# Optimization experiments

Measured on AMD Instinct MI355X. Metric: run time of the kernel, lower is better.

Reference implementation:

```python
import jax, jax.numpy as jnp
import numpy as np

N = 50000
IN_CH = 256
HID = 256
E = 800000


def setup_inputs() -> dict:
    key = jax.random.key(0)
    ks = jax.random.split(key, 12)
    s = 1.0 / np.sqrt(HID)
    return {
        "x": jax.random.normal(ks[0], (N, IN_CH), jnp.float32),
        "edge_index": jax.random.randint(ks[1], (2, E), 0, N, dtype=jnp.int64),
        "prev_embedding": jax.random.normal(ks[2], (N, HID), jnp.float32),
        "W1": jax.random.normal(ks[3], (IN_CH, HID), jnp.float32) / np.sqrt(IN_CH),
        "b1": jnp.zeros((HID,), jnp.float32),
        "W2": jax.random.normal(ks[4], (HID, HID), jnp.float32) * s,
        "b2": jnp.zeros((HID,), jnp.float32),
        "gWw": jax.random.normal(ks[5], (HID, HID), jnp.float32) * s,
        "gWb": jnp.zeros((HID,), jnp.float32),
        "gUw": jax.random.normal(ks[6], (HID, HID), jnp.float32) * s,
        "gUb": jnp.zeros((HID,), jnp.float32),
    }


def _gcn_conv(x, W, b, src, dst, norm):
    # PyG GCNConv: h = x @ W; out[i] = sum_j norm_ij * h[j]; + bias
    h = x @ W
    msg = h[src] * norm[:, None]  # [E+N, H]
    out = jax.ops.segment_sum(msg, dst, num_segments=N)
    return out + b


def _norm_and_loops(edge_index):
    loop = jnp.arange(N, dtype=edge_index.dtype)
    src = jnp.concatenate([edge_index[0], loop])
    dst = jnp.concatenate([edge_index[1], loop])
    deg = jax.ops.segment_sum(jnp.ones_like(dst, dtype=jnp.float32), dst, num_segments=N)
    dinv = jnp.where(deg > 0, jax.lax.rsqrt(deg), 0.0)
    norm = dinv[src] * dinv[dst]
    return src, dst, norm


def reference(x, edge_index, prev_embedding, W1, b1, W2, b2, gWw, gWb, gUw, gUb):
    src, dst, norm = _norm_and_loops(edge_index)
    h = jax.nn.relu(_gcn_conv(x, W1, b1, src, dst, norm))
    h_t = _gcn_conv(h, W2, b2, src, dst, norm)
    alpha = jax.nn.sigmoid(h_t @ gWw + gWb + prev_embedding @ gUw + gUb)
    h_tilde = alpha * h_t + (1.0 - alpha) * prev_embedding
    return (h_tilde, h_t)
```

## Files before the change

### kernel.cpp

```cpp
#include <hip/hip_runtime.h>
#include <hip/hip_bf16.h>
#include <math.h>

#define HIDC 256
#define LSTR 40

typedef short short8 __attribute__((ext_vector_type(8)));
typedef float f32x4 __attribute__((ext_vector_type(4)));

__device__ __forceinline__ ushort f2bf_rne(float f) {
    uint u = __float_as_uint(f);
    u += 0x7FFF + ((u >> 16) & 1);
    return (ushort)(u >> 16);
}
__device__ __forceinline__ float bf2f(ushort h) {
    return __uint_as_float(((uint)h) << 16);
}


__global__ void fill_i_kernel(int* __restrict__ p, int v, int n) {
    int i = blockIdx.x * 256 + threadIdx.x;
    if (i < n) p[i] = v;
}

__global__ void deg_kernel(const int* __restrict__ dst, int* __restrict__ deg, int E) {
    int e = blockIdx.x * 256 + threadIdx.x;
    if (e < E) atomicAdd(&deg[dst[e]], 1);
}

__global__ void rsqrt_kernel(const int* __restrict__ deg, float* __restrict__ dinv, int n) {
    int i = blockIdx.x * 256 + threadIdx.x;
    if (i < n) dinv[i] = rsqrtf((float)(deg[i] + 1));
}


__device__ __forceinline__ int block_incl_scan(int v, int tid) {
#pragma unroll
    for (int off = 1; off < 64; off <<= 1) {
        int t = __shfl_up(v, off);
        if ((tid & 63) >= off) v += t;
    }
    __shared__ int wt[4];
    if ((tid & 63) == 63) wt[tid >> 6] = v;
    __syncthreads();
    int wid = tid >> 6;
    for (int w = 0; w < wid; w++) v += wt[w];
    __syncthreads();
    return v;
}

__global__ void scan_a_kernel(const int* __restrict__ deg, int* __restrict__ row_start,
                              int* __restrict__ blocksum, int N) {
    int tid = threadIdx.x;
    int i = blockIdx.x * 256 + tid;
    int v = (i < N) ? deg[i] : 0;
    int incl = block_incl_scan(v, tid);
    if (i < N) row_start[i + 1] = incl;
    if (tid == 255) blocksum[blockIdx.x] = incl;
}

__global__ void scan_b_kernel(int* __restrict__ blocksum, int nb) {
    int tid = threadIdx.x;
    int v = (tid < nb) ? blocksum[tid] : 0;
    int incl = block_incl_scan(v, tid);
    if (tid < nb) blocksum[tid] = incl;
}

__global__ void scan_c_kernel(int* __restrict__ row_start, int* __restrict__ cursor,
                              const int* __restrict__ blocksum, int N) {
    int b = blockIdx.x;
    int i = b * 256 + threadIdx.x;
    int add = (b > 0) ? blocksum[b - 1] : 0;
    if (i < N) {
        int v = row_start[i + 1] + add;
        row_start[i + 1] = v;
        cursor[i + 1] = v;
    }
    if (b == 0 && threadIdx.x == 0) { row_start[0] = 0; cursor[0] = 0; }
}

__global__ void scatter_kernel(const int* __restrict__ src, const int* __restrict__ dst,
                               const float* __restrict__ dinv, int* __restrict__ cursor,
                               int* __restrict__ csr_src, float* __restrict__ csr_w, int E) {
    int e = blockIdx.x * 256 + threadIdx.x;
    if (e < E) {
        int s = src[e], d = dst[e];
        int pos = atomicAdd(&cursor[d], 1);
        csr_src[pos] = s;
        csr_w[pos] = dinv[s] * dinv[d];
    }
}


__global__ void prep_bt_kernel(const float* __restrict__ B, ushort* __restrict__ Bt) {
    int n = blockIdx.x, k = threadIdx.x;
    Bt[n * 256 + k] = f2bf_rne(B[k * 256 + n]);
}

__global__ void prep_gate_bt_kernel(const float* __restrict__ gWw, const float* __restrict__ gUw,
                                    ushort* __restrict__ Bth, ushort* __restrict__ Btl) {
    int n = blockIdx.x, k = threadIdx.x;
    float v1 = gWw[k * 256 + n];
    uint u1 = __float_as_uint(v1);
    Bth[n * 512 + k] = (ushort)(u1 >> 16);
    Btl[n * 512 + k] = f2bf_rne(v1 - __uint_as_float(u1 & 0xFFFF0000u));
    float v2 = gUw[k * 256 + n];
    uint u2 = __float_as_uint(v2);
    Bth[n * 512 + 256 + k] = (ushort)(u2 >> 16);
    Btl[n * 512 + 256 + k] = f2bf_rne(v2 - __uint_as_float(u2 & 0xFFFF0000u));
}


__global__ __launch_bounds__(256, 4) void gemm_bf16_kernel(
    const float* __restrict__ A, const ushort* __restrict__ Bt,
    ushort* __restrict__ C, int M)
{
    __shared__ __align__(16) ushort As[64 * LSTR];
    __shared__ __align__(16) ushort Bs[128 * LSTR];
    const int tl = threadIdx.x;
    const int lane = tl & 63, wave = tl >> 6;
    const int wm = (wave & 1) * 32, wn = (wave >> 1) * 64;
    const int bm = blockIdx.x * 64, bn = blockIdx.y * 128;

    const int arA = tl >> 2;
    const int kqA = (tl & 3) * 8;
    const int arB = tl >> 1;
    const int kqB = (tl & 1) * 16;
    const bool aok = (bm + arA) < M;

    f32x4 acc[2][4] = {};

    for (int k0 = 0; k0 < 256; k0 += 32) {
        {
            const float* ap = A + (size_t)(bm + arA) * HIDC + k0 + kqA;
            float4 v0 = aok ? *(const float4*)(ap)     : make_float4(0.f, 0.f, 0.f, 0.f);
            float4 v1 = aok ? *(const float4*)(ap + 4) : make_float4(0.f, 0.f, 0.f, 0.f);
            ushort4 h0, h1;
            h0.x = f2bf_rne(v0.x); h0.y = f2bf_rne(v0.y); h0.z = f2bf_rne(v0.z); h0.w = f2bf_rne(v0.w);
            h1.x = f2bf_rne(v1.x); h1.y = f2bf_rne(v1.y); h1.z = f2bf_rne(v1.z); h1.w = f2bf_rne(v1.w);
            *(ushort4*)&As[arA * LSTR + kqA]     = h0;
            *(ushort4*)&As[arA * LSTR + kqA + 4] = h1;
        }
        {
            const ushort* bp = Bt + (size_t)(bn + arB) * 256 + k0 + kqB;
            *(uint4*)&Bs[arB * LSTR + kqB]     = *(const uint4*)bp;
            *(uint4*)&Bs[arB * LSTR + kqB + 8] = *(const uint4*)(bp + 8);
        }
        __syncthreads();
        const int fr = lane & 15, koff = (lane >> 4) * 8;
        short8 af[2], bfv[4];
#pragma unroll
        for (int t = 0; t < 2; t++)
            af[t]  = *(const short8*)&As[(wm + t * 16 + fr) * LSTR + koff];
#pragma unroll
        for (int t = 0; t < 4; t++)
            bfv[t] = *(const short8*)&Bs[(wn + t * 16 + fr) * LSTR + koff];
#pragma unroll
        for (int mt = 0; mt < 2; mt++)
#pragma unroll
            for (int nt = 0; nt < 4; nt++)
                acc[mt][nt] = __builtin_amdgcn_mfma_f32_16x16x32_bf16(af[mt], bfv[nt], acc[mt][nt], 0, 0, 0);
        __syncthreads();
    }

    const int row4 = (lane >> 4) * 4, coln = lane & 15;
#pragma unroll
    for (int mt = 0; mt < 2; mt++)
#pragma unroll
        for (int r = 0; r < 4; r++) {
            int m = bm + wm + mt * 16 + row4 + r;
            if (m < M) {
#pragma unroll
                for (int nt = 0; nt < 4; nt++) {
                    int n = bn + wn + nt * 16 + coln;
                    C[(size_t)m * HIDC + n] = f2bf_rne(acc[mt][nt][r]);
                }
            }
        }
}


__global__ __launch_bounds__(256, 4) void gemm_bf16A_kernel(
    const ushort* __restrict__ A, const ushort* __restrict__ Bt,
    ushort* __restrict__ C, int M)
{
    __shared__ __align__(16) ushort As[64 * LSTR];
    __shared__ __align__(16) ushort Bs[128 * LSTR];
    const int tl = threadIdx.x;
    const int lane = tl & 63, wave = tl >> 6;
    const int wm = (wave & 1) * 32, wn = (wave >> 1) * 64;
    const int bm = blockIdx.x * 64, bn = blockIdx.y * 128;

    const int arA = tl >> 2;
    const int kqA = (tl & 3) * 8;
    const int arB = tl >> 1;
    const int kqB = (tl & 1) * 16;
    const bool aok = (bm + arA) < M;

    f32x4 acc[2][4] = {};

    for (int k0 = 0; k0 < 256; k0 += 32) {
        {
            const ushort* ap = A + (size_t)(bm + arA) * HIDC + k0 + kqA;
            uint2 z = make_uint2(0u, 0u);
            *(uint2*)&As[arA * LSTR + kqA]     = aok ? *(const uint2*)ap       : z;
            *(uint2*)&As[arA * LSTR + kqA + 4] = aok ? *(const uint2*)(ap + 4) : z;
        }
        {
            const ushort* bp = Bt + (size_t)(bn + arB) * 256 + k0 + kqB;
            *(uint4*)&Bs[arB * LSTR + kqB]     = *(const uint4*)bp;
            *(uint4*)&Bs[arB * LSTR + kqB + 8] = *(const uint4*)(bp + 8);
        }
        __syncthreads();
        const int fr = lane & 15, koff = (lane >> 4) * 8;
        short8 af[2], bfv[4];
#pragma unroll
        for (int t = 0; t < 2; t++)
            af[t]  = *(const short8*)&As[(wm + t * 16 + fr) * LSTR + koff];
#pragma unroll
        for (int t = 0; t < 4; t++)
            bfv[t] = *(const short8*)&Bs[(wn + t * 16 + fr) * LSTR + koff];
#pragma unroll
        for (int mt = 0; mt < 2; mt++)
#pragma unroll
            for (int nt = 0; nt < 4; nt++)
                acc[mt][nt] = __builtin_amdgcn_mfma_f32_16x16x32_bf16(af[mt], bfv[nt], acc[mt][nt], 0, 0, 0);
        __syncthreads();
    }

    const int row4 = (lane >> 4) * 4, coln = lane & 15;
#pragma unroll
    for (int mt = 0; mt < 2; mt++)
#pragma unroll
        for (int r = 0; r < 4; r++) {
            int m = bm + wm + mt * 16 + row4 + r;
            if (m < M) {
#pragma unroll
                for (int nt = 0; nt < 4; nt++) {
                    int n = bn + wn + nt * 16 + coln;
                    C[(size_t)m * HIDC + n] = f2bf_rne(acc[mt][nt][r]);
                }
            }
        }
}


__global__ __launch_bounds__(256, 4) void gate_kernel(
    const float* __restrict__ ht, const float* __restrict__ prev,
    const ushort* __restrict__ Bth, const ushort* __restrict__ Btl,
    const float* __restrict__ gWb, const float* __restrict__ gUb,
    float* __restrict__ out, int M)
{
    __shared__ __align__(16) ushort Ash[64 * LSTR];
    __shared__ __align__(16) ushort Asl[64 * LSTR];
    __shared__ __align__(16) ushort Bsh[128 * LSTR];
    __shared__ __align__(16) ushort Bsl[128 * LSTR];
    const int tl = threadIdx.x;
    const int lane = tl & 63, wave = tl >> 6;
    const int wm = (wave & 1) * 32, wn = (wave >> 1) * 64;
    const int bm = blockIdx.x * 64, bn = blockIdx.y * 128;

    const int arA = tl >> 2;
    const int kqA = (tl & 3) * 8;
    const int arB = tl >> 1;
    const int kqB = (tl & 1) * 16;
    const bool aok = (bm + arA) < M;

    f32x4 acc[2][4] = {};

    for (int k0 = 0; k0 < 512; k0 += 32) {
        {
            const float* srcA = (k0 < 256) ? ht : prev;
            const float* ap = srcA + (size_t)(bm + arA) * HIDC + (k0 & 255) + kqA;
            float4 v0 = aok ? *(const float4*)(ap)     : make_float4(0.f, 0.f, 0.f, 0.f);
            float4 v1 = aok ? *(const float4*)(ap + 4) : make_float4(0.f, 0.f, 0.f, 0.f);
            float vv[8] = {v0.x, v0.y, v0.z, v0.w, v1.x, v1.y, v1.z, v1.w};
            ushort hp[8], lp[8];
#pragma unroll
            for (int q = 0; q < 8; q++) {
                uint u = __float_as_uint(vv[q]);
                hp[q] = (ushort)(u >> 16);
                lp[q] = f2bf_rne(vv[q] - __uint_as_float(u & 0xFFFF0000u));
            }
            *(ushort4*)&Ash[arA * LSTR + kqA]     = make_ushort4(hp[0], hp[1], hp[2], hp[3]);
            *(ushort4*)&Ash[arA * LSTR + kqA + 4] = make_ushort4(hp[4], hp[5], hp[6], hp[7]);
            *(ushort4*)&Asl[arA * LSTR + kqA]     = make_ushort4(lp[0], lp[1], lp[2], lp[3]);
            *(ushort4*)&Asl[arA * LSTR + kqA + 4] = make_ushort4(lp[4], lp[5], lp[6], lp[7]);
        }
        {
            const ushort* bph = Bth + (size_t)(bn + arB) * 512 + k0 + kqB;
            const ushort* bpl = Btl + (size_t)(bn + arB) * 512 + k0 + kqB;
            *(uint4*)&Bsh[arB * LSTR + kqB]     = *(const uint4*)bph;
            *(uint4*)&Bsh[arB * LSTR + kqB + 8] = *(const uint4*)(bph + 8);
            *(uint4*)&Bsl[arB * LSTR + kqB]     = *(const uint4*)bpl;
            *(uint4*)&Bsl[arB * LSTR + kqB + 8] = *(const uint4*)(bpl + 8);
        }
        __syncthreads();
        const int fr = lane & 15, koff = (lane >> 4) * 8;
        short8 afh[2], afl[2], bfh[4], bfl[4];
#pragma unroll
        for (int t = 0; t < 2; t++) {
            afh[t] = *(const short8*)&Ash[(wm + t * 16 + fr) * LSTR + koff];
            afl[t] = *(const short8*)&Asl[(wm + t * 16 + fr) * LSTR + koff];
        }
#pragma unroll
        for (int t = 0; t < 4; t++) {
            bfh[t] = *(const short8*)&Bsh[(wn + t * 16 + fr) * LSTR + koff];
            bfl[t] = *(const short8*)&Bsl[(wn + t * 16 + fr) * LSTR + koff];
        }
#pragma unroll
        for (int mt = 0; mt < 2; mt++)
#pragma unroll
            for (int nt = 0; nt < 4; nt++) {
                acc[mt][nt] = __builtin_amdgcn_mfma_f32_16x16x32_bf16(afh[mt], bfh[nt], acc[mt][nt], 0, 0, 0);
                acc[mt][nt] = __builtin_amdgcn_mfma_f32_16x16x32_bf16(afh[mt], bfl[nt], acc[mt][nt], 0, 0, 0);
                acc[mt][nt] = __builtin_amdgcn_mfma_f32_16x16x32_bf16(afl[mt], bfh[nt], acc[mt][nt], 0, 0, 0);
            }
        __syncthreads();
    }

    const int row4 = (lane >> 4) * 4, coln = lane & 15;
#pragma unroll
    for (int mt = 0; mt < 2; mt++)
#pragma unroll
        for (int r = 0; r < 4; r++) {
            int m = bm + wm + mt * 16 + row4 + r;
            if (m < M) {
#pragma unroll
                for (int nt = 0; nt < 4; nt++) {
                    int n = bn + wn + nt * 16 + coln;
                    size_t idx = (size_t)m * HIDC + n;
                    float g = acc[mt][nt][r] + gWb[n] + gUb[n];
                    float alpha = 1.f / (1.f + expf(-g));
                    out[idx] = alpha * ht[idx] + (1.f - alpha) * prev[idx];
                }
            }
        }
}


__global__ __launch_bounds__(256) void csr_agg_kernel(
    const ushort* __restrict__ hm, const int* __restrict__ row_start,
    const int* __restrict__ csr_src, const float* __restrict__ csr_w,
    const float* __restrict__ dinv, const float* __restrict__ bias,
    float* __restrict__ outf, ushort* __restrict__ outb, int do_relu, int N)
{
    const int wave = threadIdx.x >> 6, lane = threadIdx.x & 63;
    const int i = blockIdx.x * 4 + wave;
    if (i >= N) return;
    const int c = lane * 4;

    const float di = dinv[i];
    const float s2 = di * di;
    ushort4 sv = *(const ushort4*)(hm + (size_t)i * HIDC + c);
    float a0 = s2 * bf2f(sv.x), a1 = s2 * bf2f(sv.y);
    float a2 = s2 * bf2f(sv.z), a3 = s2 * bf2f(sv.w);

    const int b0 = row_start[i], b1 = row_start[i + 1];
    int t = b0;
    for (; t + 4 <= b1; t += 4) {
        int   i0 = csr_src[t],     i1 = csr_src[t + 1];
        int   i2 = csr_src[t + 2], i3 = csr_src[t + 3];
        float w0 = csr_w[t],       w1 = csr_w[t + 1];
        float w2 = csr_w[t + 2],   w3 = csr_w[t + 3];
        ushort4 v0 = *(const ushort4*)(hm + (size_t)i0 * HIDC + c);
        ushort4 v1 = *(const ushort4*)(hm + (size_t)i1 * HIDC + c);
        ushort4 v2 = *(const ushort4*)(hm + (size_t)i2 * HIDC + c);
        ushort4 v3 = *(const ushort4*)(hm + (size_t)i3 * HIDC + c);
        a0 += w0 * bf2f(v0.x); a1 += w0 * bf2f(v0.y); a2 += w0 * bf2f(v0.z); a3 += w0 * bf2f(v0.w);
        a0 += w1 * bf2f(v1.x); a1 += w1 * bf2f(v1.y); a2 += w1 * bf2f(v1.z); a3 += w1 * bf2f(v1.w);
        a0 += w2 * bf2f(v2.x); a1 += w2 * bf2f(v2.y); a2 += w2 * bf2f(v2.z); a3 += w2 * bf2f(v2.w);
        a0 += w3 * bf2f(v3.x); a1 += w3 * bf2f(v3.y); a2 += w3 * bf2f(v3.z); a3 += w3 * bf2f(v3.w);
    }
    for (; t < b1; ++t) {
        int s_ = csr_src[t];
        float w = csr_w[t];
        ushort4 v = *(const ushort4*)(hm + (size_t)s_ * HIDC + c);
        a0 += w * bf2f(v.x); a1 += w * bf2f(v.y); a2 += w * bf2f(v.z); a3 += w * bf2f(v.w);
    }

    float4 bb = *(const float4*)(bias + c);
    a0 += bb.x; a1 += bb.y; a2 += bb.z; a3 += bb.w;
    if (do_relu) {
        a0 = fmaxf(a0, 0.f); a1 = fmaxf(a1, 0.f);
        a2 = fmaxf(a2, 0.f); a3 = fmaxf(a3, 0.f);
    }
    if (outb) {
        ushort4 o;
        o.x = f2bf_rne(a0); o.y = f2bf_rne(a1);
        o.z = f2bf_rne(a2); o.w = f2bf_rne(a3);
        *(ushort4*)(outb + (size_t)i * HIDC + c) = o;
    } else {
        *(float4*)(outf + (size_t)i * HIDC + c) = make_float4(a0, a1, a2, a3);
    }
}


extern "C" void kernel_launch(void* const* d_in, const int* in_sizes, int n_in,
                              void* d_out, int out_size, void* d_ws, size_t ws_size,
                              hipStream_t stream) {
    const float* x    = (const float*)d_in[0];
    const int*   ei   = (const int*)d_in[1];
    const float* prev = (const float*)d_in[2];
    const float* W1   = (const float*)d_in[3];
    const float* b1   = (const float*)d_in[4];
    const float* W2   = (const float*)d_in[5];
    const float* b2   = (const float*)d_in[6];
    const float* gWw  = (const float*)d_in[7];
    const float* gWb  = (const float*)d_in[8];
    const float* gUw  = (const float*)d_in[9];
    const float* gUb  = (const float*)d_in[10];

    const int N = in_sizes[0] / HIDC;
    const int E = in_sizes[1] / 2;
    const int* src = ei;
    const int* dst = ei + E;

    float* out  = (float*)d_out;
    float* out1 = out;
    float* ht   = out + (size_t)N * HIDC;
    ushort* hbf = (ushort*)out1;

    float* ws = (float*)d_ws;
    size_t o = 0;
    auto take = [&](size_t n) { size_t r = o; o += (n + 63) & ~(size_t)63; return r; };
    float*  dinv    = ws + take(N);
    int*    degi    = (int*)(ws + take(N));
    int*    row_st  = (int*)(ws + take(N + 1));
    int*    cursor  = (int*)(ws + take(N + 1));
    int*    csr_src = (int*)(ws + take(E));
    float*  csr_w   = ws + take(E);
    ushort* Bt1     = (ushort*)(ws + take(256 * 256 / 2));
    ushort* Bt2     = (ushort*)(ws + take(256 * 256 / 2));
    ushort* Bth     = (ushort*)(ws + take(256 * 512 / 2));
    ushort* Btl     = (ushort*)(ws + take(256 * 512 / 2));
    ushort* hm      = (ushort*)(ws + take((size_t)N * HIDC / 2));

    const int nbN = (N + 255) / 256;
    const int nbE = (E + 255) / 256;
    dim3 ggrid((N + 63) / 64, 2);
    const int nbAgg = (N + 3) / 4;

    int* blocksum = (int*)csr_w;
    fill_i_kernel<<<nbN, 256, 0, stream>>>(degi, 0, N);
    deg_kernel<<<nbE, 256, 0, stream>>>(dst, degi, E);
    scan_a_kernel<<<nbN, 256, 0, stream>>>(degi, row_st, blocksum, N);
    scan_b_kernel<<<1, 256, 0, stream>>>(blocksum, nbN);
    scan_c_kernel<<<nbN, 256, 0, stream>>>(row_st, cursor, blocksum, N);
    rsqrt_kernel<<<nbN, 256, 0, stream>>>(degi, dinv, N);
    scatter_kernel<<<nbE, 256, 0, stream>>>(src, dst, dinv, cursor, csr_src, csr_w, E);

    prep_bt_kernel<<<256, 256, 0, stream>>>(W1, Bt1);
    prep_bt_kernel<<<256, 256, 0, stream>>>(W2, Bt2);
    prep_gate_bt_kernel<<<256, 256, 0, stream>>>(gWw, gUw, Bth, Btl);

    gemm_bf16_kernel<<<ggrid, 256, 0, stream>>>(x, Bt1, hm, N);
    csr_agg_kernel<<<nbAgg, 256, 0, stream>>>(hm, row_st, csr_src, csr_w, dinv, b1,
                                              nullptr, hbf, 1, N);

    gemm_bf16A_kernel<<<ggrid, 256, 0, stream>>>(hbf, Bt2, hm, N);
    csr_agg_kernel<<<nbAgg, 256, 0, stream>>>(hm, row_st, csr_src, csr_w, dinv, b2,
                                              ht, nullptr, 0, N);

    gate_kernel<<<ggrid, 256, 0, stream>>>(ht, prev, Bth, Btl, gWb, gUb, out1, N);

    (void)n_in; (void)out_size; (void)ws_size;
}
```

Baseline: 516.0 us.

## Drop LDS staging in GEMMs and pre-swizzle weights into MFMA fragment layout

All three GEMM kernels stop staging A and B tiles through shared memory. Each wave now loads its A fragments straight from global memory. B fragments come from a weight buffer that the prep kernels pre-arrange into the exact per-lane MFMA operand order, so the per-K-step __syncthreads and LDS traffic go away. The cost is redundant global/L2 reads: the two waves that share rows fetch the same A data, and the waves that share columns fetch the same B data. Latency hiding also now relies on occupancy, since there is no explicit double buffering.

```diff
diff --git a/kernel.cpp b/kernel.cpp
--- a/kernel.cpp
+++ b/kernel.cpp
@@ -3,7 +3,6 @@
 #include <math.h>
 
 #define HIDC 256
-#define LSTR 40
 
 typedef short short8 __attribute__((ext_vector_type(8)));
 typedef float f32x4 __attribute__((ext_vector_type(4)));
@@ -15,6 +14,24 @@
 }
 __device__ __forceinline__ float bf2f(ushort h) {
     return __uint_as_float(((uint)h) << 16);
+}
+
+__device__ __forceinline__ short8 pack8_rne(float4 a, float4 b) {
+    ushort h[8];
+    h[0] = f2bf_rne(a.x); h[1] = f2bf_rne(a.y); h[2] = f2bf_rne(a.z); h[3] = f2bf_rne(a.w);
+    h[4] = f2bf_rne(b.x); h[5] = f2bf_rne(b.y); h[6] = f2bf_rne(b.z); h[7] = f2bf_rne(b.w);
+    return *(short8*)h;
+}
+__device__ __forceinline__ void split8(float4 a, float4 b, short8& hi, short8& lo) {
+    float v[8] = {a.x, a.y, a.z, a.w, b.x, b.y, b.z, b.w};
+    ushort hh[8], ll[8];
+#pragma unroll
+    for (int q = 0; q < 8; q++) {
+        uint u = __float_as_uint(v[q]);
+        hh[q] = (ushort)(u >> 16);
+        ll[q] = f2bf_rne(v[q] - __uint_as_float(u & 0xFFFF0000u));
+    }
+    hi = *(short8*)hh; lo = *(short8*)ll;
 }
 
 
@@ -92,75 +109,65 @@
 }
 
 
-__global__ void prep_bt_kernel(const float* __restrict__ B, ushort* __restrict__ Bt) {
+__global__ void prep_bt_kernel(const float* __restrict__ B, ushort* __restrict__ BF) {
     int n = blockIdx.x, k = threadIdx.x;
-    Bt[n * 256 + k] = f2bf_rne(B[k * 256 + n]);
+    ushort v = f2bf_rne(B[k * 256 + n]);
+    int lane = ((k >> 3) & 3) * 16 + (n & 15);
+    int idx = ((n >> 4) * 4096) + ((k >> 5) * 512) + lane * 8 + (k & 7);
+    BF[idx] = v;
 }
 
 __global__ void prep_gate_bt_kernel(const float* __restrict__ gWw, const float* __restrict__ gUw,
-                                    ushort* __restrict__ Bth, ushort* __restrict__ Btl) {
-    int n = blockIdx.x, k = threadIdx.x;
-    float v1 = gWw[k * 256 + n];
-    uint u1 = __float_as_uint(v1);
-    Bth[n * 512 + k] = (ushort)(u1 >> 16);
-    Btl[n * 512 + k] = f2bf_rne(v1 - __uint_as_float(u1 & 0xFFFF0000u));
-    float v2 = gUw[k * 256 + n];
-    uint u2 = __float_as_uint(v2);
-    Bth[n * 512 + 256 + k] = (ushort)(u2 >> 16);
-    Btl[n * 512 + 256 + k] = f2bf_rne(v2 - __uint_as_float(u2 & 0xFFFF0000u));
+                                    ushort* __restrict__ BhF, ushort* __restrict__ BlF) {
+    int n = blockIdx.x, t = threadIdx.x;
+#pragma unroll
+    for (int p = 0; p < 2; p++) {
+        int k = p * 256 + t;
+        float v = (p ? gUw : gWw)[t * 256 + n];
+        uint u = __float_as_uint(v);
+        ushort hi = (ushort)(u >> 16);
+        ushort lo = f2bf_rne(v - __uint_as_float(u & 0xFFFF0000u));
+        int lane = ((k >> 3) & 3) * 16 + (n & 15);
+        int idx = ((n >> 4) * 8192) + ((k >> 5) * 512) + lane * 8 + (k & 7);
+        BhF[idx] = hi; BlF[idx] = lo;
+    }
 }
 
 
 __global__ __launch_bounds__(256, 4) void gemm_bf16_kernel(
-    const float* __restrict__ A, const ushort* __restrict__ Bt,
+    const float* __restrict__ A, const ushort* __restrict__ BF,
     ushort* __restrict__ C, int M)
 {
-    __shared__ __align__(16) ushort As[64 * LSTR];
-    __shared__ __align__(16) ushort Bs[128 * LSTR];
     const int tl = threadIdx.x;
     const int lane = tl & 63, wave = tl >> 6;
     const int wm = (wave & 1) * 32, wn = (wave >> 1) * 64;
     const int bm = blockIdx.x * 64, bn = blockIdx.y * 128;
-
-    const int arA = tl >> 2;
-    const int kqA = (tl & 3) * 8;
-    const int arB = tl >> 1;
-    const int kqB = (tl & 1) * 16;
-    const bool aok = (bm + arA) < M;
+    const int fr = lane & 15, kg = (lane >> 4) * 8;
+
+    const int r0 = bm + wm + fr, r1 = r0 + 16;
+    const bool ok0 = r0 < M, ok1 = r1 < M;
+    const float* a0 = A + (size_t)r0 * HIDC + kg;
+    const float* a1 = A + (size_t)r1 * HIDC + kg;
+    const ushort* bp = BF + (size_t)((bn + wn) >> 4) * 4096 + lane * 8;
 
     f32x4 acc[2][4] = {};
 
-    for (int k0 = 0; k0 < 256; k0 += 32) {
-        {
-            const float* ap = A + (size_t)(bm + arA) * HIDC + k0 + kqA;
-            float4 v0 = aok ? *(const float4*)(ap)     : make_float4(0.f, 0.f, 0.f, 0.f);
-            float4 v1 = aok ? *(const float4*)(ap + 4) : make_float4(0.f, 0.f, 0.f, 0.f);
-            ushort4 h0, h1;
-            h0.x = f2bf_rne(v0.x); h0.y = f2bf_rne(v0.y); h0.z = f2bf_rne(v0.z); h0.w = f2bf_rne(v0.w);
-            h1.x = f2bf_rne(v1.x); h1.y = f2bf_rne(v1.y); h1.z = f2bf_rne(v1.z); h1.w = f2bf_rne(v1.w);
-            *(ushort4*)&As[arA * LSTR + kqA]     = h0;
-            *(ushort4*)&As[arA * LSTR + kqA + 4] = h1;
-        }
-        {
-            const ushort* bp = Bt + (size_t)(bn + arB) * 256 + k0 + kqB;
-            *(uint4*)&Bs[arB * LSTR + kqB]     = *(const uint4*)bp;
-            *(uint4*)&Bs[arB * LSTR + kqB + 8] = *(const uint4*)(bp + 8);
-        }
-        __syncthreads();
-        const int fr = lane & 15, koff = (lane >> 4) * 8;
-        short8 af[2], bfv[4];
-#pragma unroll
-        for (int t = 0; t < 2; t++)
-            af[t]  = *(const short8*)&As[(wm + t * 16 + fr) * LSTR + koff];
-#pragma unroll
-        for (int t = 0; t < 4; t++)
-            bfv[t] = *(const short8*)&Bs[(wn + t * 16 + fr) * LSTR + koff];
-#pragma unroll
-        for (int mt = 0; mt < 2; mt++)
-#pragma unroll
-            for (int nt = 0; nt < 4; nt++)
-                acc[mt][nt] = __builtin_amdgcn_mfma_f32_16x16x32_bf16(af[mt], bfv[nt], acc[mt][nt], 0, 0, 0);
-        __syncthreads();
+    for (int kq = 0; kq < 8; kq++) {
+        float4 z = make_float4(0.f, 0.f, 0.f, 0.f);
+        float4 u0 = z, u1 = z, v0 = z, v1 = z;
+        if (ok0) { u0 = *(const float4*)(a0 + kq * 32); u1 = *(const float4*)(a0 + kq * 32 + 4); }
+        if (ok1) { v0 = *(const float4*)(a1 + kq * 32); v1 = *(const float4*)(a1 + kq * 32 + 4); }
+        short8 af0 = pack8_rne(u0, u1);
+        short8 af1 = pack8_rne(v0, v1);
+        short8 bfv[4];
+#pragma unroll
+        for (int nt = 0; nt < 4; nt++)
+            bfv[nt] = *(const short8*)(bp + ((size_t)nt * 8 + kq) * 512);
+#pragma unroll
+        for (int nt = 0; nt < 4; nt++) {
+            acc[0][nt] = __builtin_amdgcn_mfma_f32_16x16x32_bf16(af0, bfv[nt], acc[0][nt], 0, 0, 0);
+            acc[1][nt] = __builtin_amdgcn_mfma_f32_16x16x32_bf16(af1, bfv[nt], acc[1][nt], 0, 0, 0);
+        }
     }
 
     const int row4 = (lane >> 4) * 4, coln = lane & 15;
@@ -181,51 +188,36 @@
 
 
 __global__ __launch_bounds__(256, 4) void gemm_bf16A_kernel(
-    const ushort* __restrict__ A, const ushort* __restrict__ Bt,
+    const ushort* __restrict__ A, const ushort* __restrict__ BF,
     ushort* __restrict__ C, int M)
 {
-    __shared__ __align__(16) ushort As[64 * LSTR];
-    __shared__ __align__(16) ushort Bs[128 * LSTR];
     const int tl = threadIdx.x;
     const int lane = tl & 63, wave = tl >> 6;
     const int wm = (wave & 1) * 32, wn = (wave >> 1) * 64;
     const int bm = blockIdx.x * 64, bn = blockIdx.y * 128;
-
-    const int arA = tl >> 2;
-    const int kqA = (tl & 3) * 8;
-    const int arB = tl >> 1;
-    const int kqB = (tl & 1) * 16;
-    const bool aok = (bm + arA) < M;
+    const int fr = lane & 15, kg = (lane >> 4) * 8;
+
+    const int r0 = bm + wm + fr, r1 = r0 + 16;
+    const bool ok0 = r0 < M, ok1 = r1 < M;
+    const ushort* a0 = A + (size_t)r0 * HIDC + kg;
+    const ushort* a1 = A + (size_t)r1 * HIDC + kg;
+    const ushort* bp = BF + (size_t)((bn + wn) >> 4) * 4096 + lane * 8;
 
     f32x4 acc[2][4] = {};
 
-    for (int k0 = 0; k0 < 256; k0 += 32) {
-        {
-            const ushort* ap = A + (size_t)(bm + arA) * HIDC + k0 + kqA;
-            uint2 z = make_uint2(0u, 0u);
-            *(uint2*)&As[arA * LSTR + kqA]     = aok ? *(const uint2*)ap       : z;
-            *(uint2*)&As[arA * LSTR + kqA + 4] = aok ? *(const uint2*)(ap + 4) : z;
-        }
-        {
-            const ushort* bp = Bt + (size_t)(bn + arB) * 256 + k0 + kqB;
-            *(uint4*)&Bs[arB * LSTR + kqB]     = *(const uint4*)bp;
-            *(uint4*)&Bs[arB * LSTR + kqB + 8] = *(const uint4*)(bp + 8);
-        }
-        __syncthreads();
-        const int fr = lane & 15, koff = (lane >> 4) * 8;
-        short8 af[2], bfv[4];
-#pragma unroll
-        for (int t = 0; t < 2; t++)
-            af[t]  = *(const short8*)&As[(wm + t * 16 + fr) * LSTR + koff];
-#pragma unroll
-        for (int t = 0; t < 4; t++)
-            bfv[t] = *(const short8*)&Bs[(wn + t * 16 + fr) * LSTR + koff];
-#pragma unroll
-        for (int mt = 0; mt < 2; mt++)
-#pragma unroll
-            for (int nt = 0; nt < 4; nt++)
-                acc[mt][nt] = __builtin_amdgcn_mfma_f32_16x16x32_bf16(af[mt], bfv[nt], acc[mt][nt], 0, 0, 0);
-        __syncthreads();
+    for (int kq = 0; kq < 8; kq++) {
+        short8 af0 = {}, af1 = {};
+        if (ok0) af0 = *(const short8*)(a0 + kq * 32);
+        if (ok1) af1 = *(const short8*)(a1 + kq * 32);
+        short8 bfv[4];
+#pragma unroll
+        for (int nt = 0; nt < 4; nt++)
+            bfv[nt] = *(const short8*)(bp + ((size_t)nt * 8 + kq) * 512);
+#pragma unroll
+        for (int nt = 0; nt < 4; nt++) {
+            acc[0][nt] = __builtin_amdgcn_mfma_f32_16x16x32_bf16(af0, bfv[nt], acc[0][nt], 0, 0, 0);
+            acc[1][nt] = __builtin_amdgcn_mfma_f32_16x16x32_bf16(af1, bfv[nt], acc[1][nt], 0, 0, 0);
+        }
     }
 
     const int row4 = (lane >> 4) * 4, coln = lane & 15;
@@ -247,76 +239,51 @@
 
 __global__ __launch_bounds__(256, 4) void gate_kernel(
     const float* __restrict__ ht, const float* __restrict__ prev,
-    const ushort* __restrict__ Bth, const ushort* __restrict__ Btl,
+    const ushort* __restrict__ BhF, const ushort* __restrict__ BlF,
     const float* __restrict__ gWb, const float* __restrict__ gUb,
     float* __restrict__ out, int M)
 {
-    __shared__ __align__(16) ushort Ash[64 * LSTR];
-    __shared__ __align__(16) ushort Asl[64 * LSTR];
-    __shared__ __align__(16) ushort Bsh[128 * LSTR];
-    __shared__ __align__(16) ushort Bsl[128 * LSTR];
     const int tl = threadIdx.x;
     const int lane = tl & 63, wave = tl >> 6;
     const int wm = (wave & 1) * 32, wn = (wave >> 1) * 64;
     const int bm = blockIdx.x * 64, bn = blockIdx.y * 128;
-
-    const int arA = tl >> 2;
-    const int kqA = (tl & 3) * 8;
-    const int arB = tl >> 1;
-    const int kqB = (tl & 1) * 16;
-    const bool aok = (bm + arA) < M;
+    const int fr = lane & 15, kg = (lane >> 4) * 8;
+
+    const int r0 = bm + wm + fr, r1 = r0 + 16;
+    const bool ok0 = r0 < M, ok1 = r1 < M;
+    const size_t ro0 = (size_t)r0 * HIDC + kg;
+    const size_t ro1 = (size_t)r1 * HIDC + kg;
+    const ushort* bph = BhF + (size_t)((bn + wn) >> 4) * 8192 + lane * 8;
+    const ushort* bpl = BlF + (size_t)((bn + wn) >> 4) * 8192 + lane * 8;
 
     f32x4 acc[2][4] = {};
 
-    for (int k0 = 0; k0 < 512; k0 += 32) {
-        {
-            const float* srcA = (k0 < 256) ? ht : prev;
-            const float* ap = srcA + (size_t)(bm + arA) * HIDC + (k0 & 255) + kqA;
-            float4 v0 = aok ? *(const float4*)(ap)     : make_float4(0.f, 0.f, 0.f, 0.f);
-            float4 v1 = aok ? *(const float4*)(ap + 4) : make_float4(0.f, 0.f, 0.f, 0.f);
-            float vv[8] = {v0.x, v0.y, v0.z, v0.w, v1.x, v1.y, v1.z, v1.w};
-            ushort hp[8], lp[8];
-#pragma unroll
-            for (int q = 0; q < 8; q++) {
-                uint u = __float_as_uint(vv[q]);
-                hp[q] = (ushort)(u >> 16);
-                lp[q] = f2bf_rne(vv[q] - __uint_as_float(u & 0xFFFF0000u));
-            }
-            *(ushort4*)&Ash[arA * LSTR + kqA]     = make_ushort4(hp[0], hp[1], hp[2], hp[3]);
-            *(ushort4*)&Ash[arA * LSTR + kqA + 4] = make_ushort4(hp[4], hp[5], hp[6], hp[7]);
-            *(ushort4*)&Asl[arA * LSTR + kqA]     = make_ushort4(lp[0], lp[1], lp[2], lp[3]);
-            *(ushort4*)&Asl[arA * LSTR + kqA + 4] = make_ushort4(lp[4], lp[5], lp[6], lp[7]);
-        }
-        {
-            const ushort* bph = Bth + (size_t)(bn + arB) * 512 + k0 + kqB;
-            const ushort* bpl = Btl + (size_t)(bn + arB) * 512 + k0 + kqB;
-            *(uint4*)&Bsh[arB * LSTR + kqB]     = *(const uint4*)bph;
-            *(uint4*)&Bsh[arB * LSTR + kqB + 8] = *(const uint4*)(bph + 8);
-            *(uint4*)&Bsl[arB * LSTR + kqB]     = *(const uint4*)bpl;
-            *(uint4*)&Bsl[arB * LSTR + kqB + 8] = *(const uint4*)(bpl + 8);
-        }
-        __syncthreads();
-        const int fr = lane & 15, koff = (lane >> 4) * 8;
-        short8 afh[2], afl[2], bfh[4], bfl[4];
-#pragma unroll
-        for (int t = 0; t < 2; t++) {
-            afh[t] = *(const short8*)&Ash[(wm + t * 16 + fr) * LSTR + koff];
-            afl[t] = *(const short8*)&Asl[(wm + t * 16 + fr) * LSTR + koff];
-        }
-#pragma unroll
-        for (int t = 0; t < 4; t++) {
-            bfh[t] = *(const short8*)&Bsh[(wn + t * 16 + fr) * LSTR + koff];
-            bfl[t] = *(const short8*)&Bsl[(wn + t * 16 + fr) * LSTR + koff];
-        }
-#pragma unroll
-        for (int mt = 0; mt < 2; mt++)
-#pragma unroll
-            for (int nt = 0; nt < 4; nt++) {
-                acc[mt][nt] = __builtin_amdgcn_mfma_f32_16x16x32_bf16(afh[mt], bfh[nt], acc[mt][nt], 0, 0, 0);
-                acc[mt][nt] = __builtin_amdgcn_mfma_f32_16x16x32_bf16(afh[mt], bfl[nt], acc[mt][nt], 0, 0, 0);
-                acc[mt][nt] = __builtin_amdgcn_mfma_f32_16x16x32_bf16(afl[mt], bfh[nt], acc[mt][nt], 0, 0, 0);
-            }
-        __syncthreads();
+    for (int kq = 0; kq < 16; kq++) {
+        const float* S = (kq < 8) ? ht : prev;
+        const int cb = (kq & 7) * 32;
+        float4 z = make_float4(0.f, 0.f, 0.f, 0.f);
+        float4 u0 = z, u1 = z, v0 = z, v1 = z;
+        if (ok0) { u0 = *(const float4*)(S + ro0 + cb); u1 = *(const float4*)(S + ro0 + cb + 4); }
+        if (ok1) { v0 = *(const float4*)(S + ro1 + cb); v1 = *(const float4*)(S + ro1 + cb + 4); }
+        short8 ah0, al0, ah1, al1;
+        split8(u0, u1, ah0, al0);
+        split8(v0, v1, ah1, al1);
+        short8 bfh[4], bfl[4];
+#pragma unroll
+        for (int nt = 0; nt < 4; nt++) {
+            size_t off = ((size_t)nt * 16 + kq) * 512;
+            bfh[nt] = *(const short8*)(bph + off);
+            bfl[nt] = *(const short8*)(bpl + off);
+        }
+#pragma unroll
+        for (int nt = 0; nt < 4; nt++) {
+            acc[0][nt] = __builtin_amdgcn_mfma_f32_16x16x32_bf16(ah0, bfh[nt], acc[0][nt], 0, 0, 0);
+            acc[0][nt] = __builtin_amdgcn_mfma_f32_16x16x32_bf16(ah0, bfl[nt], acc[0][nt], 0, 0, 0);
+            acc[0][nt] = __builtin_amdgcn_mfma_f32_16x16x32_bf16(al0, bfh[nt], acc[0][nt], 0, 0, 0);
+            acc[1][nt] = __builtin_amdgcn_mfma_f32_16x16x32_bf16(ah1, bfh[nt], acc[1][nt], 0, 0, 0);
+            acc[1][nt] = __builtin_amdgcn_mfma_f32_16x16x32_bf16(ah1, bfl[nt], acc[1][nt], 0, 0, 0);
+            acc[1][nt] = __builtin_amdgcn_mfma_f32_16x16x32_bf16(al1, bfh[nt], acc[1][nt], 0, 0, 0);
+        }
     }
 
     const int row4 = (lane >> 4) * 4, coln = lane & 15;
@@ -430,10 +397,10 @@
     int*    cursor  = (int*)(ws + take(N + 1));
     int*    csr_src = (int*)(ws + take(E));
     float*  csr_w   = ws + take(E);
-    ushort* Bt1     = (ushort*)(ws + take(256 * 256 / 2));
-    ushort* Bt2     = (ushort*)(ws + take(256 * 256 / 2));
-    ushort* Bth     = (ushort*)(ws + take(256 * 512 / 2));
-    ushort* Btl     = (ushort*)(ws + take(256 * 512 / 2));
+    ushort* Bt1F    = (ushort*)(ws + take(256 * 256 / 2));
+    ushort* Bt2F    = (ushort*)(ws + take(256 * 256 / 2));
+    ushort* BthF    = (ushort*)(ws + take(256 * 512 / 2));
+    ushort* BtlF    = (ushort*)(ws + take(256 * 512 / 2));
     ushort* hm      = (ushort*)(ws + take((size_t)N * HIDC / 2));
 
     const int nbN = (N + 255) / 256;
@@ -450,19 +417,19 @@
     rsqrt_kernel<<<nbN, 256, 0, stream>>>(degi, dinv, N);
     scatter_kernel<<<nbE, 256, 0, stream>>>(src, dst, dinv, cursor, csr_src, csr_w, E);
 
-    prep_bt_kernel<<<256, 256, 0, stream>>>(W1, Bt1);
-    prep_bt_kernel<<<256, 256, 0, stream>>>(W2, Bt2);
-    prep_gate_bt_kernel<<<256, 256, 0, stream>>>(gWw, gUw, Bth, Btl);
-
-    gemm_bf16_kernel<<<ggrid, 256, 0, stream>>>(x, Bt1, hm, N);
+    prep_bt_kernel<<<256, 256, 0, stream>>>(W1, Bt1F);
+    prep_bt_kernel<<<256, 256, 0, stream>>>(W2, Bt2F);
+    prep_gate_bt_kernel<<<256, 256, 0, stream>>>(gWw, gUw, BthF, BtlF);
+
+    gemm_bf16_kernel<<<ggrid, 256, 0, stream>>>(x, Bt1F, hm, N);
     csr_agg_kernel<<<nbAgg, 256, 0, stream>>>(hm, row_st, csr_src, csr_w, dinv, b1,
                                               nullptr, hbf, 1, N);
 
-    gemm_bf16A_kernel<<<ggrid, 256, 0, stream>>>(hbf, Bt2, hm, N);
+    gemm_bf16A_kernel<<<ggrid, 256, 0, stream>>>(hbf, Bt2F, hm, N);
     csr_agg_kernel<<<nbAgg, 256, 0, stream>>>(hm, row_st, csr_src, csr_w, dinv, b2,
                                               ht, nullptr, 0, N);
 
-    gate_kernel<<<ggrid, 256, 0, stream>>>(ht, prev, Bth, Btl, gWb, gUb, out1, N);
+    gate_kernel<<<ggrid, 256, 0, stream>>>(ht, prev, BthF, BtlF, gWb, gUb, out1, N);
 
     (void)n_in; (void)out_size; (void)ws_size;
 }
```

Result: slower. 567.3 us (+10.0%).
